# Kernel tuning notes

Measured on AMD Instinct MI355X. Metric: run time of the kernel, lower is better.

## Reference

```python
import jax, jax.numpy as jnp
import numpy as np

D_MODEL = 1024
N_HEADS = 16
D_K = D_MODEL // N_HEADS


def setup_inputs() -> dict:
    key = jax.random.key(0)
    ks = jax.random.split(key, 16)
    B, S = 2, 2048
    sc = 1.0 / np.sqrt(D_MODEL)
    inp = {
        "query": jax.random.normal(ks[0], (B, S, D_MODEL), jnp.float32),
        "key": jax.random.normal(ks[1], (B, S, D_MODEL), jnp.float32),
        "value": jax.random.normal(ks[2], (B, S, D_MODEL), jnp.float32),
        "Wq": jax.random.normal(ks[3], (D_MODEL, D_MODEL), jnp.float32) * sc,
        "bq": jnp.zeros((D_MODEL,), jnp.float32),
        "Wk": jax.random.normal(ks[4], (D_MODEL, D_MODEL), jnp.float32) * sc,
        "bk": jnp.zeros((D_MODEL,), jnp.float32),
        "Wv": jax.random.normal(ks[5], (D_MODEL, D_MODEL), jnp.float32) * sc,
        "bv": jnp.zeros((D_MODEL,), jnp.float32),
        "Wo": jax.random.normal(ks[6], (D_MODEL, D_MODEL), jnp.float32) * sc,
        "bo": jnp.zeros((D_MODEL,), jnp.float32),
        "theta": jax.random.normal(ks[7], (N_HEADS,), jnp.float32) * 0.1,
        "gate": jax.random.normal(ks[8], (D_MODEL,), jnp.float32) * 0.1,
    }
    return inp


def reference(query, key, value, Wq, bq, Wk, bk, Wv, bv, Wo, bo, theta, gate):
    B, Sq, D = query.shape
    Sk = key.shape[1]
    # linear projections (torch Linear: x @ W.T + b), split heads -> [B,H,S,d_k]
    Q = (query @ Wq.T + bq).reshape(B, Sq, N_HEADS, D_K).transpose(0, 2, 1, 3)
    K = (key @ Wk.T + bk).reshape(B, Sk, N_HEADS, D_K).transpose(0, 2, 1, 3)
    V = (value @ Wv.T + bv).reshape(B, Sk, N_HEADS, D_K).transpose(0, 2, 1, 3)

    inv_sqrt_dk = 1.0 / jnp.sqrt(jnp.float32(D_K))
    scores = jnp.einsum("bhqd,bhkd->bhqk", Q, K) * inv_sqrt_dk

    # per-head rotation of the first two feature dims of Q
    cos_t = jnp.cos(theta)[None, :, None, None]  # [1,H,1,1]
    sin_t = jnp.sin(theta)[None, :, None, None]
    q_rot = jnp.concatenate(
        [
            cos_t * Q[..., :1] - sin_t * Q[..., 1:2],
            sin_t * Q[..., :1] + cos_t * Q[..., 1:2],
            Q[..., 2:],
        ],
        axis=-1,
    )
    scores_q = jnp.einsum("bhqd,bhkd->bhqk", q_rot, K) * inv_sqrt_dk

    g_scalar = jax.nn.sigmoid(gate.mean())
    scores = g_scalar * scores_q + (1.0 - g_scalar) * scores

    attn = jax.nn.softmax(scores, axis=-1)
    out = jnp.einsum("bhqk,bhkd->bhqd", attn, V)
    out = out.transpose(0, 2, 1, 3).reshape(B, Sq, D)
    return out @ Wo.T + bo
```

## Files before the change

### kernel.cpp

```cpp
#include <hip/hip_runtime.h>


typedef __bf16 bf16;
typedef __attribute__((ext_vector_type(8))) bf16 bf16x8;
typedef __attribute__((ext_vector_type(4))) bf16 bf16x4;
typedef __attribute__((ext_vector_type(2))) bf16 bf16x2;
typedef __attribute__((ext_vector_type(4))) float f32x4;
typedef unsigned int u32;

#define D_MODEL 1024
#define NH 16
#define DKH 64
#define SEQ 2048

#define GLL16(g, l) __builtin_amdgcn_global_load_lds(                      \
    (const __attribute__((address_space(1))) void*)(g),                    \
    (__attribute__((address_space(3))) void*)(l), 16, 0, 0)

static __device__ __forceinline__ f32x4 mfma16(bf16x8 a, bf16x8 b, f32x4 c) {
  return __builtin_amdgcn_mfma_f32_16x16x32_bf16(a, b, c, 0, 0, 0);
}

static __device__ __forceinline__ u32 pk2(float a, float b) {
  bf16x2 v; v[0] = (bf16)a; v[1] = (bf16)b;
  return __builtin_bit_cast(u32, v);
}

static __device__ __forceinline__ float fexp2(float x) {
#if __has_builtin(__builtin_amdgcn_exp2f)
  return __builtin_amdgcn_exp2f(x);
#else
  return exp2f(x);
#endif
}

#define CQK 0.1803368801111244f
#define MSHIFT 12.0f

__global__ __launch_bounds__(256) void prep(const float* __restrict__ query,
                                            const float* __restrict__ key,
                                            const float* __restrict__ value,
                                            const float* __restrict__ Wq,
                                            const float* __restrict__ bq,
                                            const float* __restrict__ Wk,
                                            const float* __restrict__ Wv,
                                            const float* __restrict__ Wo,
                                            const float* __restrict__ gate,
                                            const float* __restrict__ theta,
                                            bf16* __restrict__ Xq,
                                            bf16* __restrict__ Xk,
                                            bf16* __restrict__ Xv,
                                            bf16* __restrict__ Wqp,
                                            bf16* __restrict__ Wkp,
                                            bf16* __restrict__ Wvp,
                                            bf16* __restrict__ Wop,
                                            float* __restrict__ bqp) {
  const int id = blockIdx.x;
  const int tid = threadIdx.x;
  if (id >= 4096) {
    const int rem = id - 4096;
    const int iz = rem >> 12;
    const int ib = rem & 4095;
    const float* s = (iz == 0) ? query : (iz == 1) ? key : value;
    bf16* d = (iz == 0) ? Xq : (iz == 1) ? Xk : Xv;
    const size_t i = (size_t)(ib * 256 + tid) * 4;
    float4 w = *(const float4*)(s + i);
    bf16x4 o; o[0] = (bf16)w.x; o[1] = (bf16)w.y; o[2] = (bf16)w.z; o[3] = (bf16)w.w;
    *(bf16x4*)(d + i) = o;
    return;
  }
  const int wz = id >> 10, wb = id & 1023;
  if (wz != 0) {
    const float* s = (wz == 1) ? Wk : (wz == 2) ? Wv : Wo;
    bf16* dd = (wz == 1) ? Wkp : (wz == 2) ? Wvp : Wop;
    const size_t i = (size_t)(wb * 256 + tid) * 4;
    float4 v = *(const float4*)(s + i);
    bf16x4 o4; o4[0] = (bf16)v.x; o4[1] = (bf16)v.y; o4[2] = (bf16)v.z; o4[3] = (bf16)v.w;
    *(bf16x4*)(dd + i) = o4;
    return;
  }
  __shared__ float red[4];
  float ssum = 0.f;
  for (int i = tid; i < D_MODEL; i += 256) ssum += gate[i];
#pragma unroll
  for (int off = 32; off > 0; off >>= 1) ssum += __shfl_down(ssum, off);
  if ((tid & 63) == 0) red[tid >> 6] = ssum;
  __syncthreads();
  const float g = 1.f / (1.f + __expf(-(red[0] + red[1] + red[2] + red[3]) / 1024.f));

  const int t = wb * 256 + tid;
  const int r = t >> 8;
  const int c0 = (t & 255) * 4;
  const int d = r & 63, h = r >> 6;
  float4 w = *(const float4*)(Wq + (size_t)r * D_MODEL + c0);
  float4 o;
  if (d == 0) {
    const float a = (g * cosf(theta[h]) + (1.f - g)) * CQK;
    const float bb = (g * sinf(theta[h])) * CQK;
    float4 w2 = *(const float4*)(Wq + (size_t)(r + 1) * D_MODEL + c0);
    o.x = a * w.x - bb * w2.x; o.y = a * w.y - bb * w2.y;
    o.z = a * w.z - bb * w2.z; o.w = a * w.w - bb * w2.w;
    if (c0 == 0) bqp[r] = a * bq[r] - bb * bq[r + 1];
  } else if (d == 1) {
    const float a = (g * cosf(theta[h]) + (1.f - g)) * CQK;
    const float bb = (g * sinf(theta[h])) * CQK;
    float4 w2 = *(const float4*)(Wq + (size_t)(r - 1) * D_MODEL + c0);
    o.x = bb * w2.x + a * w.x; o.y = bb * w2.y + a * w.y;
    o.z = bb * w2.z + a * w.z; o.w = bb * w2.w + a * w.w;
    if (c0 == 0) bqp[r] = bb * bq[r - 1] + a * bq[r];
  } else {
    o.x = CQK * w.x; o.y = CQK * w.y;
    o.z = CQK * w.z; o.w = CQK * w.w;
    if (c0 == 0) bqp[r] = CQK * bq[r];
  }
  bf16x4 ov; ov[0] = (bf16)o.x; ov[1] = (bf16)o.y; ov[2] = (bf16)o.z; ov[3] = (bf16)o.w;
  *(bf16x4*)(Wqp + (size_t)r * D_MODEL + c0) = ov;
}

static __device__ __forceinline__ void gemm_bt_main(const bf16* __restrict__ A,
                                                    const bf16* __restrict__ Bt,
                                                    int tm, int tn, int K,
                                                    f32x4 acc[4][4]) {
  __shared__ bf16 lA[8192];
  __shared__ bf16 lB[8192];
  const int tid = threadIdx.x;
  const int lane = tid & 63, wv = tid >> 6;
  const int wm = wv >> 1, wn = wv & 1;
  const int l16 = lane & 15, lg = lane >> 4;

#pragma unroll
  for (int i = 0; i < 4; ++i)
#pragma unroll
    for (int j = 0; j < 4; ++j) acc[i][j] = (f32x4){0.f, 0.f, 0.f, 0.f};

  int offA[4][2], offB[4][2];
#pragma unroll
  for (int f = 0; f < 4; ++f)
#pragma unroll
    for (int kc = 0; kc < 2; ++kc) {
      const int m = wm * 64 + f * 16 + l16;
      offA[f][kc] = m * 64 + (((kc * 4 + lg) ^ (m & 7)) << 3);
      const int n = wn * 64 + f * 16 + l16;
      offB[f][kc] = n * 64 + (((kc * 4 + lg) ^ (n & 7)) << 3);
    }

  const int rowb = tid >> 3, oct = tid & 7;
  const int soct = oct ^ (rowb & 7);
  const bf16* gA[4];
  const bf16* gB[4];
#pragma unroll
  for (int rd = 0; rd < 4; ++rd) {
    gA[rd] = A + (size_t)(tm + rd * 32 + rowb) * K + soct * 8;
    gB[rd] = Bt + (size_t)(tn + rd * 32 + rowb) * K + soct * 8;
  }

  for (int kt = 0; kt < K; kt += 64) {
    __syncthreads();
#pragma unroll
    for (int rd = 0; rd < 4; ++rd) {
      GLL16(gA[rd] + kt, &lA[rd * 2048 + wv * 512]);
      GLL16(gB[rd] + kt, &lB[rd * 2048 + wv * 512]);
    }
    __syncthreads();
#pragma unroll
    for (int kc = 0; kc < 2; ++kc) {
      bf16x8 af[4], bv[4];
#pragma unroll
      for (int f = 0; f < 4; ++f) {
        af[f] = *(const bf16x8*)&lA[offA[f][kc]];
        bv[f] = *(const bf16x8*)&lB[offB[f][kc]];
      }
#pragma unroll
      for (int i = 0; i < 4; ++i)
#pragma unroll
        for (int j = 0; j < 4; ++j)
          acc[i][j] = mfma16(af[i], bv[j], acc[i][j]);
    }
  }
}

__global__ __launch_bounds__(256) void gemm_qkv(
    const bf16* __restrict__ Xq, const bf16* __restrict__ Xk, const bf16* __restrict__ Xv,
    const bf16* __restrict__ Wq, const bf16* __restrict__ Wk, const bf16* __restrict__ Wv,
    const float* __restrict__ bqp, const float* __restrict__ bk, const float* __restrict__ bv,
    bf16* __restrict__ Qp, bf16* __restrict__ Kp, bf16* __restrict__ Vt) {
  const int wgp = (blockIdx.x & 7) * 96 + (blockIdx.x >> 3);
  const int z = wgp >> 8;
  const int rem = wgp & 255;
  const int tm = (rem >> 3) * 128, tn = (rem & 7) * 128;
  const bf16* A = (z == 0) ? Xq : (z == 1) ? Xk : Xv;
  const bf16* Bt = (z == 0) ? Wq : (z == 1) ? Wk : Wv;
  const float* bias = (z == 0) ? bqp : (z == 1) ? bk : bv;
  f32x4 acc[4][4];
  gemm_bt_main(A, Bt, tm, tn, D_MODEL, acc);
  const int lane = threadIdx.x & 63, wv = threadIdx.x >> 6;
  const int wm = wv >> 1, wn = wv & 1, l16 = lane & 15, lg = lane >> 4;
  if (z < 2) {
    bf16* C = (z == 0) ? Qp : Kp;
#pragma unroll
    for (int i = 0; i < 4; ++i) {
      const int m0 = tm + wm * 64 + i * 16 + lg * 4;
#pragma unroll
      for (int j = 0; j < 4; ++j) {
        const int n = tn + wn * 64 + j * 16 + l16;
        const float bb = bias[n];
        const int h = n >> 6, d = n & 63;
#pragma unroll
        for (int r = 0; r < 4; ++r) {
          const int m = m0 + r;
          const int b = m >> 11, s = m & 2047;
          C[((size_t)(b * NH + h) * SEQ + s) * DKH + d] = (bf16)(acc[i][j][r] + bb);
        }
      }
    }
  } else {
#pragma unroll
    for (int i = 0; i < 4; ++i) {
      const int m0 = tm + wm * 64 + i * 16 + lg * 4;
      const int b = m0 >> 11, s0 = m0 & 2047;
#pragma unroll
      for (int j = 0; j < 4; ++j) {
        const int n = tn + wn * 64 + j * 16 + l16;
        const float bb = bias[n];
        const int h = n >> 6, d = n & 63;
        bf16x4 ov;
#pragma unroll
        for (int r = 0; r < 4; ++r) ov[r] = (bf16)(acc[i][j][r] + bb);
        *(bf16x4*)&Vt[((size_t)(b * NH + h) * DKH + d) * SEQ + s0] = ov;
      }
    }
  }
}

__global__ __launch_bounds__(256) void gemm_out_k(const bf16* __restrict__ A,
                                                  const bf16* __restrict__ Bt,
                                                  const float* __restrict__ bias,
                                                  float* __restrict__ C) {
  const int wgp = (blockIdx.x & 7) * 32 + (blockIdx.x >> 3);
  const int tm = (wgp >> 3) * 128, tn = (wgp & 7) * 128;
  f32x4 acc[4][4];
  gemm_bt_main(A, Bt, tm, tn, D_MODEL, acc);
  const int lane = threadIdx.x & 63, wv = threadIdx.x >> 6;
  const int wm = wv >> 1, wn = wv & 1, l16 = lane & 15, lg = lane >> 4;
#pragma unroll
  for (int i = 0; i < 4; ++i) {
    const int m0 = tm + wm * 64 + i * 16 + lg * 4;
#pragma unroll
    for (int j = 0; j < 4; ++j) {
      const int n = tn + wn * 64 + j * 16 + l16;
      const float bb = bias[n];
#pragma unroll
      for (int r = 0; r < 4; ++r)
        C[(size_t)(m0 + r) * D_MODEL + n] = acc[i][j][r] + bb;
    }
  }
}

__global__ __launch_bounds__(512, 4) void attn_kernel(const bf16* __restrict__ Qp,
                                                      const bf16* __restrict__ Kp,
                                                      const bf16* __restrict__ Vt,
                                                      bf16* __restrict__ Op) {
  __shared__ __align__(16) bf16 lK0[8192];
  __shared__ __align__(16) bf16 lV0[8192];
  __shared__ __align__(16) bf16 lK1[8192];
  __shared__ __align__(16) bf16 lV1[8192];
  __shared__ __align__(16) bf16 lP[8192];

  const int tid = threadIdx.x;
  const int lane = tid & 63, w = tid >> 6;
  const int l16 = lane & 15, lg = lane >> 4;
  const int qg = w >> 1, kg = w & 1;
  const int wgp = (blockIdx.x & 7) * 64 + (blockIdx.x >> 3);
  const int bh = wgp >> 4;
  const int b = bh >> 4, h = bh & 15;
  const int q0 = (wgp & 15) * 128;
  const int qw0 = q0 + qg * 32;
  const size_t kvb = (size_t)bh * SEQ * DKH;

  bf16x8 aq[2][2];
#pragma unroll
  for (int qq = 0; qq < 2; ++qq)
#pragma unroll
    for (int kc = 0; kc < 2; ++kc)
      aq[qq][kc] = *(const bf16x8*)&Qp[kvb +
          (size_t)(qw0 + qq * 16 + l16) * DKH + kc * 32 + lg * 8];

  f32x4 o[2][4];
#pragma unroll
  for (int qq = 0; qq < 2; ++qq)
#pragma unroll
    for (int dt = 0; dt < 4; ++dt) o[qq][dt] = (f32x4){0.f, 0.f, 0.f, 0.f};
  f32x4 lacc[2];
  lacc[0] = (f32x4){0.f, 0.f, 0.f, 0.f};
  lacc[1] = (f32x4){0.f, 0.f, 0.f, 0.f};

  bf16x8 ones;
#pragma unroll
  for (int j = 0; j < 8; ++j) ones[j] = (bf16)1.0f;

  const int kr = tid >> 3, oct = tid & 7;
  const bf16* gKs = Kp + kvb + (size_t)kr * DKH + (oct ^ (kr & 7)) * 8;
  const bf16* gKs2 = gKs + (size_t)64 * DKH;
  const int vd = tid >> 4, vsc = tid & 15;
  const bf16* gVs = Vt + kvb + (size_t)vd * SEQ + ((vsc ^ (vd & 7)) * 8);
  const bf16* gVs2 = gVs + (size_t)32 * SEQ;

  bf16* lPw = &lP[w * 1024];
  int pwr[2][2];
#pragma unroll
  for (int fn = 0; fn < 2; ++fn)
#pragma unroll
    for (int qq = 0; qq < 2; ++qq)
      pwr[fn][qq] = l16 * 64 + (((qq * 4 + fn * 2 + (lg >> 1)) ^ (l16 & 7)) << 3) +
                    ((lg & 1) << 2);
  int prd[2];
#pragma unroll
  for (int qq = 0; qq < 2; ++qq)
    prd[qq] = l16 * 64 + (((qq * 4 + lg) ^ (l16 & 7)) << 3);

  auto stageTile = [&](bf16* dK, bf16* dV, int t) {
    const size_t ko = (size_t)t * 128 * DKH;
    const int vo = t * 128;
    GLL16(gKs + ko, dK + tid * 8);
    GLL16(gKs2 + ko, dK + tid * 8 + 4096);
    GLL16(gVs + vo, dV + tid * 8);
    GLL16(gVs2 + vo, dV + tid * 8 + 4096);
  };

  auto computeTile = [&](const bf16* K, const bf16* V) {
#pragma unroll
    for (int ss = 0; ss < 2; ++ss) {
      f32x4 st[2][2];
      __builtin_amdgcn_s_setprio(1);
#pragma unroll
      for (int fn = 0; fn < 2; ++fn) {
        const int row = ss * 64 + kg * 32 + fn * 16 + l16;
        bf16x8 ka = *(const bf16x8*)&K[row * 64 + ((lg ^ (row & 7)) << 3)];
        bf16x8 kb = *(const bf16x8*)&K[row * 64 + (((4 + lg) ^ (row & 7)) << 3)];
#pragma unroll
        for (int qq = 0; qq < 2; ++qq) {
          f32x4 tt = (f32x4){0.f, 0.f, 0.f, 0.f};
          tt = mfma16(ka, aq[qq][0], tt);
          tt = mfma16(kb, aq[qq][1], tt);
          st[fn][qq] = tt;
        }
      }
      __builtin_amdgcn_s_setprio(0);

#pragma unroll
      for (int fn = 0; fn < 2; ++fn)
#pragma unroll
        for (int qq = 0; qq < 2; ++qq) {
          uint2 pw;
          pw.x = pk2(fexp2(st[fn][qq][0] - MSHIFT), fexp2(st[fn][qq][1] - MSHIFT));
          pw.y = pk2(fexp2(st[fn][qq][2] - MSHIFT), fexp2(st[fn][qq][3] - MSHIFT));
          *(uint2*)&lPw[pwr[fn][qq]] = pw;
        }

      bf16x8 pa0 = *(const bf16x8*)&lPw[prd[0]];
      bf16x8 pa1 = *(const bf16x8*)&lPw[prd[1]];

      __builtin_amdgcn_s_setprio(1);
      lacc[0] = mfma16(pa0, ones, lacc[0]);
      lacc[1] = mfma16(pa1, ones, lacc[1]);
#pragma unroll
      for (int dt = 0; dt < 4; ++dt) {
        const int n = dt * 16 + l16;
        bf16x8 vv = *(const bf16x8*)&V[n * 128 +
                                      (((ss * 8 + kg * 4 + lg) ^ (n & 7)) << 3)];
        o[0][dt] = mfma16(pa0, vv, o[0][dt]);
        o[1][dt] = mfma16(pa1, vv, o[1][dt]);
      }
      __builtin_amdgcn_s_setprio(0);
    }
  };

  stageTile(lK0, lV0, 0);
  __syncthreads();

  const int NT = SEQ / 128;
  for (int t = 0; t < NT; t += 2) {
    if (t + 1 < NT) stageTile(lK1, lV1, t + 1);
    computeTile(lK0, lV0);
    __syncthreads();
    if (t + 2 < NT) stageTile(lK0, lV0, t + 2);
    computeTile(lK1, lV1);
    __syncthreads();
  }

  float* cmb0 = (float*)lK0;
  float* cmb1 = (float*)lK1;
  float* cl = (float*)lP;
  float* cmb = (qg < 2) ? (cmb0 + (size_t)qg * 2048) : (cmb1 + (size_t)(qg - 2) * 2048);
  if (kg == 1) {
#pragma unroll
    for (int qq = 0; qq < 2; ++qq)
#pragma unroll
      for (int dt = 0; dt < 4; ++dt)
        *(f32x4*)&cmb[((qq * 4 + dt) * 16 + l16) * 16 + lg * 4] = o[qq][dt];
    if (l16 == 0) {
#pragma unroll
      for (int qq = 0; qq < 2; ++qq)
#pragma unroll
        for (int r = 0; r < 4; ++r)
          cl[(qg * 2 + qq) * 16 + lg * 4 + r] = lacc[qq][r];
    }
  }
  __syncthreads();
  if (kg == 0) {
#pragma unroll
    for (int qq = 0; qq < 2; ++qq) {
#pragma unroll
      for (int dt = 0; dt < 4; ++dt) {
        f32x4 p = *(const f32x4*)&cmb[((qq * 4 + dt) * 16 + l16) * 16 + lg * 4];
        o[qq][dt][0] += p[0]; o[qq][dt][1] += p[1];
        o[qq][dt][2] += p[2]; o[qq][dt][3] += p[3];
      }
      float linv[4];
#pragma unroll
      for (int r = 0; r < 4; ++r)
        linv[r] = 1.f / (lacc[qq][r] + cl[(qg * 2 + qq) * 16 + lg * 4 + r]);
#pragma unroll
      for (int r = 0; r < 4; ++r) {
        const int q = qw0 + qq * 16 + lg * 4 + r;
#pragma unroll
        for (int dt = 0; dt < 4; ++dt) {
          const int d = dt * 16 + l16;
          Op[((size_t)(b * SEQ + q)) * D_MODEL + h * DKH + d] =
              (bf16)(o[qq][dt][r] * linv[r]);
        }
      }
    }
  }
}

extern "C" void kernel_launch(void* const* d_in, const int* in_sizes, int n_in,
                              void* d_out, int out_size, void* d_ws, size_t ws_size,
                              hipStream_t stream) {
  (void)in_sizes; (void)n_in; (void)out_size; (void)ws_size;
  const float* query = (const float*)d_in[0];
  const float* key   = (const float*)d_in[1];
  const float* value = (const float*)d_in[2];
  const float* Wq    = (const float*)d_in[3];
  const float* bq    = (const float*)d_in[4];
  const float* Wk    = (const float*)d_in[5];
  const float* bk    = (const float*)d_in[6];
  const float* Wv    = (const float*)d_in[7];
  const float* bv    = (const float*)d_in[8];
  const float* Wo    = (const float*)d_in[9];
  const float* bo    = (const float*)d_in[10];
  const float* theta = (const float*)d_in[11];
  const float* gate  = (const float*)d_in[12];

  float* bqp = (float*)d_ws;
  bf16* wb = (bf16*)((char*)d_ws + 8192);
  bf16* Xq  = wb;
  bf16* Xk  = Xq + 4194304;
  bf16* Xv  = Xk + 4194304;
  bf16* Wqp = Xv + 4194304;
  bf16* Wkp = Wqp + 1048576;
  bf16* Wvp = Wkp + 1048576;
  bf16* Wop = Wvp + 1048576;
  bf16* Qp  = Wop + 1048576;
  bf16* Kp  = Qp + 4194304;
  bf16* Vt  = Kp + 4194304;
  bf16* Op  = Vt + 4194304;

  prep<<<16384, 256, 0, stream>>>(query, key, value, Wq, bq, Wk, Wv, Wo,
                                  gate, theta, Xq, Xk, Xv,
                                  Wqp, Wkp, Wvp, Wop, bqp);
  gemm_qkv<<<768, 256, 0, stream>>>(Xq, Xk, Xv, Wqp, Wkp, Wvp,
                                    bqp, bk, bv, Qp, Kp, Vt);
  attn_kernel<<<512, 512, 0, stream>>>(Qp, Kp, Vt, Op);
  gemm_out_k<<<256, 256, 0, stream>>>(Op, Wop, bo, (float*)d_out);
}
```

Measured before the change: 121.2 us.

## Halve attention tile sizes to 64 queries and 64-key chunks, double grid

The attention kernel now gives each workgroup 64 queries instead of 128, with each wave covering 16 query rows. K/V tiles are streamed in 64-key chunks instead of 128, and the grid doubles to 1024 workgroups. Shared memory per block drops by half and register use per wave falls, so launch_bounds now asks for higher occupancy. In exchange each K/V tile is reused by fewer queries, which doubles K/V global traffic and the number of barriers.

```diff
diff --git a/kernel.cpp b/kernel.cpp
--- a/kernel.cpp
+++ b/kernel.cpp
@@ -256,43 +256,36 @@
   }
 }
 
-__global__ __launch_bounds__(512, 4) void attn_kernel(const bf16* __restrict__ Qp,
+__global__ __launch_bounds__(512, 8) void attn_kernel(const bf16* __restrict__ Qp,
                                                       const bf16* __restrict__ Kp,
                                                       const bf16* __restrict__ Vt,
                                                       bf16* __restrict__ Op) {
-  __shared__ __align__(16) bf16 lK0[8192];
-  __shared__ __align__(16) bf16 lV0[8192];
-  __shared__ __align__(16) bf16 lK1[8192];
-  __shared__ __align__(16) bf16 lV1[8192];
-  __shared__ __align__(16) bf16 lP[8192];
+  __shared__ __align__(16) bf16 lK0[4096];
+  __shared__ __align__(16) bf16 lV0[4096];
+  __shared__ __align__(16) bf16 lK1[4096];
+  __shared__ __align__(16) bf16 lV1[4096];
+  __shared__ __align__(16) bf16 lP[4096];
 
   const int tid = threadIdx.x;
   const int lane = tid & 63, w = tid >> 6;
   const int l16 = lane & 15, lg = lane >> 4;
   const int qg = w >> 1, kg = w & 1;
-  const int wgp = (blockIdx.x & 7) * 64 + (blockIdx.x >> 3);
-  const int bh = wgp >> 4;
+  const int wgp = (blockIdx.x & 7) * 128 + (blockIdx.x >> 3);
+  const int bh = wgp >> 5;
   const int b = bh >> 4, h = bh & 15;
-  const int q0 = (wgp & 15) * 128;
-  const int qw0 = q0 + qg * 32;
+  const int q0 = (wgp & 31) * 64;
+  const int qw0 = q0 + qg * 16;
   const size_t kvb = (size_t)bh * SEQ * DKH;
 
-  bf16x8 aq[2][2];
-#pragma unroll
-  for (int qq = 0; qq < 2; ++qq)
-#pragma unroll
-    for (int kc = 0; kc < 2; ++kc)
-      aq[qq][kc] = *(const bf16x8*)&Qp[kvb +
-          (size_t)(qw0 + qq * 16 + l16) * DKH + kc * 32 + lg * 8];
-
-  f32x4 o[2][4];
-#pragma unroll
-  for (int qq = 0; qq < 2; ++qq)
-#pragma unroll
-    for (int dt = 0; dt < 4; ++dt) o[qq][dt] = (f32x4){0.f, 0.f, 0.f, 0.f};
-  f32x4 lacc[2];
-  lacc[0] = (f32x4){0.f, 0.f, 0.f, 0.f};
-  lacc[1] = (f32x4){0.f, 0.f, 0.f, 0.f};
+  bf16x8 aq[2];
+#pragma unroll
+  for (int kc = 0; kc < 2; ++kc)
+    aq[kc] = *(const bf16x8*)&Qp[kvb + (size_t)(qw0 + l16) * DKH + kc * 32 + lg * 8];
+
+  f32x4 o[4];
+#pragma unroll
+  for (int dt = 0; dt < 4; ++dt) o[dt] = (f32x4){0.f, 0.f, 0.f, 0.f};
+  f32x4 lacc = (f32x4){0.f, 0.f, 0.f, 0.f};
 
   bf16x8 ones;
 #pragma unroll
@@ -300,85 +293,61 @@
 
   const int kr = tid >> 3, oct = tid & 7;
   const bf16* gKs = Kp + kvb + (size_t)kr * DKH + (oct ^ (kr & 7)) * 8;
-  const bf16* gKs2 = gKs + (size_t)64 * DKH;
-  const int vd = tid >> 4, vsc = tid & 15;
-  const bf16* gVs = Vt + kvb + (size_t)vd * SEQ + ((vsc ^ (vd & 7)) * 8);
-  const bf16* gVs2 = gVs + (size_t)32 * SEQ;
-
-  bf16* lPw = &lP[w * 1024];
-  int pwr[2][2];
+  const bf16* gVs = Vt + kvb + (size_t)kr * SEQ + (oct ^ (kr & 7)) * 8;
+  bf16* lPq = &lP[qg * 1024];
+  int pwr[2];
 #pragma unroll
   for (int fn = 0; fn < 2; ++fn)
-#pragma unroll
-    for (int qq = 0; qq < 2; ++qq)
-      pwr[fn][qq] = l16 * 64 + (((qq * 4 + fn * 2 + (lg >> 1)) ^ (l16 & 7)) << 3) +
-                    ((lg & 1) << 2);
-  int prd[2];
-#pragma unroll
-  for (int qq = 0; qq < 2; ++qq)
-    prd[qq] = l16 * 64 + (((qq * 4 + lg) ^ (l16 & 7)) << 3);
+    pwr[fn] = l16 * 64 + (((kg * 4 + fn * 2 + (lg >> 1)) ^ (l16 & 7)) << 3) +
+              ((lg & 1) << 2);
+  const int prd = l16 * 64 + (((kg * 4 + lg) ^ (l16 & 7)) << 3);
 
   auto stageTile = [&](bf16* dK, bf16* dV, int t) {
-    const size_t ko = (size_t)t * 128 * DKH;
-    const int vo = t * 128;
+    const size_t ko = (size_t)t * 64 * DKH;
+    const int vo = t * 64;
     GLL16(gKs + ko, dK + tid * 8);
-    GLL16(gKs2 + ko, dK + tid * 8 + 4096);
     GLL16(gVs + vo, dV + tid * 8);
-    GLL16(gVs2 + vo, dV + tid * 8 + 4096);
   };
 
   auto computeTile = [&](const bf16* K, const bf16* V) {
-#pragma unroll
-    for (int ss = 0; ss < 2; ++ss) {
-      f32x4 st[2][2];
-      __builtin_amdgcn_s_setprio(1);
-#pragma unroll
-      for (int fn = 0; fn < 2; ++fn) {
-        const int row = ss * 64 + kg * 32 + fn * 16 + l16;
-        bf16x8 ka = *(const bf16x8*)&K[row * 64 + ((lg ^ (row & 7)) << 3)];
-        bf16x8 kb = *(const bf16x8*)&K[row * 64 + (((4 + lg) ^ (row & 7)) << 3)];
-#pragma unroll
-        for (int qq = 0; qq < 2; ++qq) {
-          f32x4 tt = (f32x4){0.f, 0.f, 0.f, 0.f};
-          tt = mfma16(ka, aq[qq][0], tt);
-          tt = mfma16(kb, aq[qq][1], tt);
-          st[fn][qq] = tt;
-        }
-      }
-      __builtin_amdgcn_s_setprio(0);
-
-#pragma unroll
-      for (int fn = 0; fn < 2; ++fn)
-#pragma unroll
-        for (int qq = 0; qq < 2; ++qq) {
-          uint2 pw;
-          pw.x = pk2(fexp2(st[fn][qq][0] - MSHIFT), fexp2(st[fn][qq][1] - MSHIFT));
-          pw.y = pk2(fexp2(st[fn][qq][2] - MSHIFT), fexp2(st[fn][qq][3] - MSHIFT));
-          *(uint2*)&lPw[pwr[fn][qq]] = pw;
-        }
-
-      bf16x8 pa0 = *(const bf16x8*)&lPw[prd[0]];
-      bf16x8 pa1 = *(const bf16x8*)&lPw[prd[1]];
-
-      __builtin_amdgcn_s_setprio(1);
-      lacc[0] = mfma16(pa0, ones, lacc[0]);
-      lacc[1] = mfma16(pa1, ones, lacc[1]);
-#pragma unroll
-      for (int dt = 0; dt < 4; ++dt) {
-        const int n = dt * 16 + l16;
-        bf16x8 vv = *(const bf16x8*)&V[n * 128 +
-                                      (((ss * 8 + kg * 4 + lg) ^ (n & 7)) << 3)];
-        o[0][dt] = mfma16(pa0, vv, o[0][dt]);
-        o[1][dt] = mfma16(pa1, vv, o[1][dt]);
-      }
-      __builtin_amdgcn_s_setprio(0);
-    }
+    f32x4 st[2];
+    __builtin_amdgcn_s_setprio(1);
+#pragma unroll
+    for (int fn = 0; fn < 2; ++fn) {
+      const int row = kg * 32 + fn * 16 + l16;
+      bf16x8 ka = *(const bf16x8*)&K[row * 64 + ((lg ^ (row & 7)) << 3)];
+      bf16x8 kb = *(const bf16x8*)&K[row * 64 + (((4 + lg) ^ (row & 7)) << 3)];
+      f32x4 tt = (f32x4){0.f, 0.f, 0.f, 0.f};
+      tt = mfma16(ka, aq[0], tt);
+      tt = mfma16(kb, aq[1], tt);
+      st[fn] = tt;
+    }
+    __builtin_amdgcn_s_setprio(0);
+
+#pragma unroll
+    for (int fn = 0; fn < 2; ++fn) {
+      uint2 pw;
+      pw.x = pk2(fexp2(st[fn][0] - MSHIFT), fexp2(st[fn][1] - MSHIFT));
+      pw.y = pk2(fexp2(st[fn][2] - MSHIFT), fexp2(st[fn][3] - MSHIFT));
+      *(uint2*)&lPq[pwr[fn]] = pw;
+    }
+    bf16x8 pa = *(const bf16x8*)&lPq[prd];
+
+    __builtin_amdgcn_s_setprio(1);
+    lacc = mfma16(pa, ones, lacc);
+#pragma unroll
+    for (int dt = 0; dt < 4; ++dt) {
+      const int n = dt * 16 + l16;
+      bf16x8 vv = *(const bf16x8*)&V[n * 64 + (((kg * 4 + lg) ^ (n & 7)) << 3)];
+      o[dt] = mfma16(pa, vv, o[dt]);
+    }
+    __builtin_amdgcn_s_setprio(0);
   };
 
   stageTile(lK0, lV0, 0);
   __syncthreads();
 
-  const int NT = SEQ / 128;
+  const int NT = SEQ / 64;
   for (int t = 0; t < NT; t += 2) {
     if (t + 1 < NT) stageTile(lK1, lV1, t + 1);
     computeTile(lK0, lV0);
@@ -388,47 +357,39 @@
     __syncthreads();
   }
 
-  float* cmb0 = (float*)lK0;
-  float* cmb1 = (float*)lK1;
+  float* cmb = (qg == 0) ? (float*)lK0 : (qg == 1) ? (float*)lV0
+             : (qg == 2) ? (float*)lK1 : (float*)lV1;
   float* cl = (float*)lP;
-  float* cmb = (qg < 2) ? (cmb0 + (size_t)qg * 2048) : (cmb1 + (size_t)(qg - 2) * 2048);
   if (kg == 1) {
 #pragma unroll
-    for (int qq = 0; qq < 2; ++qq)
-#pragma unroll
-      for (int dt = 0; dt < 4; ++dt)
-        *(f32x4*)&cmb[((qq * 4 + dt) * 16 + l16) * 16 + lg * 4] = o[qq][dt];
+    for (int dt = 0; dt < 4; ++dt)
+      *(f32x4*)&cmb[(dt * 16 + l16) * 16 + lg * 4] = o[dt];
     if (l16 == 0) {
 #pragma unroll
-      for (int qq = 0; qq < 2; ++qq)
-#pragma unroll
-        for (int r = 0; r < 4; ++r)
-          cl[(qg * 2 + qq) * 16 + lg * 4 + r] = lacc[qq][r];
+      for (int r = 0; r < 4; ++r)
+        cl[qg * 16 + lg * 4 + r] = lacc[r];
     }
   }
   __syncthreads();
   if (kg == 0) {
 #pragma unroll
-    for (int qq = 0; qq < 2; ++qq) {
+    for (int dt = 0; dt < 4; ++dt) {
+      f32x4 p = *(const f32x4*)&cmb[(dt * 16 + l16) * 16 + lg * 4];
+      o[dt][0] += p[0]; o[dt][1] += p[1];
+      o[dt][2] += p[2]; o[dt][3] += p[3];
+    }
+    float linv[4];
+#pragma unroll
+    for (int r = 0; r < 4; ++r)
+      linv[r] = 1.f / (lacc[r] + cl[qg * 16 + lg * 4 + r]);
+#pragma unroll
+    for (int r = 0; r < 4; ++r) {
+      const int q = qw0 + lg * 4 + r;
 #pragma unroll
       for (int dt = 0; dt < 4; ++dt) {
-        f32x4 p = *(const f32x4*)&cmb[((qq * 4 + dt) * 16 + l16) * 16 + lg * 4];
-        o[qq][dt][0] += p[0]; o[qq][dt][1] += p[1];
-        o[qq][dt][2] += p[2]; o[qq][dt][3] += p[3];
-      }
-      float linv[4];
-#pragma unroll
-      for (int r = 0; r < 4; ++r)
-        linv[r] = 1.f / (lacc[qq][r] + cl[(qg * 2 + qq) * 16 + lg * 4 + r]);
-#pragma unroll
-      for (int r = 0; r < 4; ++r) {
-        const int q = qw0 + qq * 16 + lg * 4 + r;
-#pragma unroll
-        for (int dt = 0; dt < 4; ++dt) {
-          const int d = dt * 16 + l16;
-          Op[((size_t)(b * SEQ + q)) * D_MODEL + h * DKH + d] =
-              (bf16)(o[qq][dt][r] * linv[r]);
-        }
+        const int d = dt * 16 + l16;
+        Op[((size_t)(b * SEQ + q)) * D_MODEL + h * DKH + d] =
+            (bf16)(o[dt][r] * linv[r]);
       }
     }
   }
@@ -471,6 +432,6 @@
                                   Wqp, Wkp, Wvp, Wop, bqp);
   gemm_qkv<<<768, 256, 0, stream>>>(Xq, Xk, Xv, Wqp, Wkp, Wvp,
                                     bqp, bk, bv, Qp, Kp, Vt);
-  attn_kernel<<<512, 512, 0, stream>>>(Qp, Kp, Vt, Op);
+  attn_kernel<<<1024, 512, 0, stream>>>(Qp, Kp, Vt, Op);
   gemm_out_k<<<256, 256, 0, stream>>>(Op, Wop, bo, (float*)d_out);
 }
```

New measurement: 138.3 us. 1.14x slower.
